# Optimization experiments

Measured on AMD Instinct MI355X. Metric: run time of the kernel, lower is better.

The kernel has to match this reference:

```python
import jax, jax.numpy as jnp
import numpy as np

IN_DIM = 1024
OUT_DIM = 1024
NUM_HEADS = 16
DEPTH = IN_DIM // NUM_HEADS  # 64


def setup_inputs() -> dict:
    key = jax.random.key(0)
    ks = jax.random.split(key, 11)
    B, S = 8, 1024  # S must equal IN_DIM (reshape constraint in original module)
    s_in = 1.0 / np.sqrt(IN_DIM)
    return {
        "query": jax.random.normal(ks[0], (B, S, IN_DIM), jnp.float32),
        "key": jax.random.normal(ks[1], (B, S, IN_DIM), jnp.float32),
        "value": jax.random.normal(ks[2], (B, S, IN_DIM), jnp.float32),
        "Wq": jax.random.normal(ks[3], (IN_DIM, IN_DIM), jnp.float32) * s_in,
        "bq": jnp.zeros((IN_DIM,), jnp.float32),
        "Wk": jax.random.normal(ks[4], (IN_DIM, IN_DIM), jnp.float32) * s_in,
        "bk": jnp.zeros((IN_DIM,), jnp.float32),
        "Wv": jax.random.normal(ks[5], (IN_DIM, IN_DIM), jnp.float32) * s_in,
        "bv": jnp.zeros((IN_DIM,), jnp.float32),
        "Wo": jax.random.normal(ks[6], (OUT_DIM, IN_DIM), jnp.float32) * s_in,
        "bo": jnp.zeros((OUT_DIM,), jnp.float32),
    }


def reference(query, key, value, Wq, bq, Wk, bk, Wv, bv, Wo, bo):
    B, S, D = query.shape
    H, P = NUM_HEADS, DEPTH

    def split_heads(x):
        # (B,S,D) -> (B,S,H,P) -> transpose last two dims -> (B,S,P,H)
        return x.reshape(B, S, H, P).swapaxes(-1, -2)

    Q = split_heads(query @ Wq.T + bq)   # (B,S,P,H)
    K = split_heads(key @ Wk.T + bk)     # (B,S,P,H)
    V = split_heads(value @ Wv.T + bv)   # (B,S,P,H)

    scale = jnp.sqrt(jnp.float32(P))
    # scores over the depth axis, per (batch, token): (B,S,P,P)
    scores = jnp.einsum('bsph,bsqh->bspq', Q, K) / scale
    # original uses softmax over dim=0 (the batch axis) - reproduce faithfully
    attn = jax.nn.softmax(scores, axis=0)
    out = jnp.einsum('bspq,bsqh->bsph', attn, V)   # (B,S,P,H)
    # transpose(-1,-2) -> (B,S,H,P), reshape to (B,S,S) (requires H*P == S)
    out = out.swapaxes(-1, -2).reshape(B, S, S)
    out = out @ Wo.T + bo                           # (B,S,OUT_DIM)
    return jax.nn.sigmoid(out)
```

## Files before the change

### kernel.cpp

```cpp
#include <hip/hip_runtime.h>


using short8   = __attribute__((ext_vector_type(8))) short;
using floatx4  = __attribute__((ext_vector_type(4))) float;
using floatx16 = __attribute__((ext_vector_type(16))) float;

__device__ __forceinline__ float bf2f(unsigned short u) {
    return __uint_as_float(((unsigned)u) << 16);
}
__device__ __forceinline__ unsigned short f2bf(float f) {
    unsigned u = __float_as_uint(f);
    u += 0x7fffu + ((u >> 16) & 1u);
    return (unsigned short)(u >> 16);
}
__device__ __forceinline__ unsigned pack_trunc(float f0, float f1) {
    return __builtin_amdgcn_perm(__float_as_uint(f1), __float_as_uint(f0), 0x07060302u);
}
__device__ __forceinline__ unsigned pack_rne(float f0, float f1) {
    return (unsigned)f2bf(f0) | ((unsigned)f2bf(f1) << 16);
}
__device__ __forceinline__ void async_ld16(const void* g, void* l) {
    __builtin_amdgcn_global_load_lds(
        (const __attribute__((address_space(1))) unsigned int*)g,
        (__attribute__((address_space(3))) unsigned int*)l, 16, 0, 0);
}
__device__ __forceinline__ short8 lds_read_b128(unsigned addr) {
    short8 r;
    asm volatile("ds_read_b128 %0, %1" : "=v"(r) : "v"(addr));
    return r;
}

__device__ __forceinline__ void conv8(const float* src, unsigned short* d, size_t i) {
    float4 a = *(const float4*)(src + i);
    float4 b = *(const float4*)(src + i + 4);
    uint4 o;
    o.x = pack_rne(a.x, a.y);
    o.y = pack_rne(a.z, a.w);
    o.z = pack_rne(b.x, b.y);
    o.w = pack_rne(b.z, b.w);
    *(uint4*)(d + i) = o;
}

__global__ __launch_bounds__(256) void convert_weights(
    const float* __restrict__ w0, const float* __restrict__ w1,
    const float* __restrict__ w2, const float* __restrict__ w3,
    unsigned short* __restrict__ dst)
{
    const float* srcs[4] = {w0, w1, w2, w3};
    conv8(srcs[blockIdx.y], dst + (size_t)blockIdx.y * (1024u * 1024u),
          ((size_t)blockIdx.x * 256 + threadIdx.x) * 8);
}

__global__ __launch_bounds__(256) void convert_acts(
    const float* __restrict__ a0, const float* __restrict__ a1,
    const float* __restrict__ a2, unsigned short* __restrict__ dst)
{
    const float* srcs[3] = {a0, a1, a2};
    conv8(srcs[blockIdx.y], dst + (size_t)blockIdx.y * ((size_t)8192 * 1024),
          ((size_t)blockIdx.x * 256 + threadIdx.x) * 8);
}

template<bool AF32, bool SIG>
__global__ __launch_bounds__(256) void gemm128(
    const void* __restrict__ A0, const void* __restrict__ A1, const void* __restrict__ A2,
    const unsigned short* __restrict__ W0, const unsigned short* __restrict__ W1,
    const unsigned short* __restrict__ W2,
    const float* __restrict__ b0, const float* __restrict__ b1, const float* __restrict__ b2,
    void* __restrict__ C0, void* __restrict__ C1, void* __restrict__ C2)
{
    const int z = blockIdx.z;
    const void* Ap = (z == 0) ? A0 : (z == 1) ? A1 : A2;
    const unsigned short* W = (z == 0) ? W0 : (z == 1) ? W1 : W2;
    const float* bias = (z == 0) ? b0 : (z == 1) ? b1 : b2;
    void* Cp = (z == 0) ? C0 : (z == 1) ? C1 : C2;

    constexpr int Kd = 1024, Nd = 1024;
    const int t = threadIdx.x;
    const int w = t >> 6, lane = t & 63;
    const int l15 = lane & 15, quad = lane >> 4;
    const int blockM = blockIdx.x * 128;
    const int blockN = blockIdx.y * 128;
    const int wy = w >> 1, wx = w & 1;

    __shared__ unsigned short Bs[128 * 32];
    constexpr int ABYTES = AF32 ? (128 * 32 * 4) : (128 * 32 * 2);
    __shared__ __align__(16) unsigned char AsRaw[ABYTES];
    float* AsF = (float*)AsRaw;
    unsigned short* AsB = (unsigned short*)AsRaw;

    const int br  = lane >> 2;
    const int bg  = (lane & 3) ^ (br & 3);
    const unsigned short* Bsrc0 = W + (size_t)(blockN + w * 32 + br) * Kd + bg * 8;
    const unsigned short* Bsrc1 = Bsrc0 + (size_t)16 * Kd;
    unsigned short* Bdst0 = &Bs[(w * 2 + 0) * 512];
    unsigned short* Bdst1 = &Bs[(w * 2 + 1) * 512];

    const int ar = lane >> 3;
    const int ag = (lane & 7) ^ (ar & 7);
    const float* AsrcF[4];
    float* AdstF[4];
    const unsigned short* AsrcB0 = nullptr; const unsigned short* AsrcB1 = nullptr;
    unsigned short* AdstB0 = nullptr; unsigned short* AdstB1 = nullptr;
    if (AF32) {
        #pragma unroll
        for (int j = 0; j < 4; ++j) {
            AsrcF[j] = (const float*)Ap + (size_t)(blockM + w * 32 + j * 8 + ar) * Kd + ag * 4;
            AdstF[j] = AsF + (w * 4 + j) * 256;
        }
    } else {
        AsrcB0 = (const unsigned short*)Ap + (size_t)(blockM + w * 32 + br) * Kd + bg * 8;
        AsrcB1 = AsrcB0 + (size_t)16 * Kd;
        AdstB0 = &AsB[(w * 2 + 0) * 512];
        AdstB1 = &AsB[(w * 2 + 1) * 512];
    }

    floatx4 acc[4][4] = {};

    for (int k0 = 0; k0 < Kd; k0 += 32) {
        if (AF32) {
            #pragma unroll
            for (int j = 0; j < 4; ++j) async_ld16(AsrcF[j] + k0, AdstF[j]);
        } else {
            async_ld16(AsrcB0 + k0, AdstB0);
            async_ld16(AsrcB1 + k0, AdstB1);
        }
        async_ld16(Bsrc0 + k0, Bdst0);
        async_ld16(Bsrc1 + k0, Bdst1);
        __syncthreads();

        short8 af[4], bfr[4];
        #pragma unroll
        for (int mt = 0; mt < 4; ++mt) {
            const int row = wy * 64 + mt * 16 + l15;
            if (AF32) {
                const int r7 = l15 & 7;
                const float* ap = AsF + row * 32;
                float4 lo = *(const float4*)(ap + (((quad * 2 + 0) ^ r7) * 4));
                float4 hi = *(const float4*)(ap + (((quad * 2 + 1) ^ r7) * 4));
                union { unsigned u[4]; short8 s; } cv;
                cv.u[0] = pack_rne(lo.x, lo.y);
                cv.u[1] = pack_rne(lo.z, lo.w);
                cv.u[2] = pack_rne(hi.x, hi.y);
                cv.u[3] = pack_rne(hi.z, hi.w);
                af[mt] = cv.s;
            } else {
                af[mt] = *(const short8*)&AsB[row * 32 + (quad ^ (l15 & 3)) * 8];
            }
        }
        #pragma unroll
        for (int nt = 0; nt < 4; ++nt) {
            const int row = wx * 64 + nt * 16 + l15;
            bfr[nt] = *(const short8*)&Bs[row * 32 + (quad ^ (l15 & 3)) * 8];
        }
        #pragma unroll
        for (int mt = 0; mt < 4; ++mt)
            #pragma unroll
            for (int nt = 0; nt < 4; ++nt)
                acc[mt][nt] = __builtin_amdgcn_mfma_f32_16x16x32_bf16(af[mt], bfr[nt], acc[mt][nt], 0, 0, 0);
        __syncthreads();
    }

    #pragma unroll
    for (int nt = 0; nt < 4; ++nt) {
        const int col = blockN + wx * 64 + nt * 16 + l15;
        const float bv = bias[col];
        #pragma unroll
        for (int mt = 0; mt < 4; ++mt) {
            const int row = blockM + wy * 64 + mt * 16 + quad * 4;
            #pragma unroll
            for (int r = 0; r < 4; ++r) {
                float v = acc[mt][nt][r] + bv;
                if (SIG) {
                    v = 1.0f / (1.0f + __expf(-v));
                    ((float*)Cp)[(size_t)(row + r) * Nd + col] = v;
                } else {
                    ((unsigned short*)Cp)[(size_t)(row + r) * Nd + col] = f2bf(v);
                }
            }
        }
    }
}

#define VMW10 do { asm volatile("s_waitcnt vmcnt(10)" ::: "memory"); } while (0)
#define VMW8  do { asm volatile("s_waitcnt vmcnt(8)"  ::: "memory"); } while (0)
#define VMW4  do { asm volatile("s_waitcnt vmcnt(4)"  ::: "memory"); } while (0)
#define VMW0  do { asm volatile("s_waitcnt vmcnt(0)"  ::: "memory"); } while (0)
#define LGKM0 do { asm volatile("s_waitcnt lgkmcnt(0)" ::: "memory"); \
                   __builtin_amdgcn_sched_barrier(0); } while (0)
#define BARRIER __builtin_amdgcn_s_barrier()

#define STG_A(BUF, KH, KE) do { \
    async_ld16(pA[0] + (KE), &lds[(BUF)*32768 + (KH)*16384 + dstW]); \
    async_ld16(pA[1] + (KE), &lds[(BUF)*32768 + (KH)*16384 + 8192 + dstW]); \
} while (0)
#define STG_B(BUF, KH, KE) do { \
    async_ld16(pB[0] + (KE), &lds[65536 + (BUF)*32768 + (KH)*16384 + dstW]); \
    async_ld16(pB[1] + (KE), &lds[65536 + (BUF)*32768 + (KH)*16384 + 8192 + dstW]); \
} while (0)

#define RD_A(BUF, KH, MH) do { \
    const unsigned rbA_ = (BUF)*32768u + (KH)*16384u; \
    aF[0][0] = lds_read_b128(aRd[(MH)*2+0][0] + rbA_); \
    aF[0][1] = lds_read_b128(aRd[(MH)*2+0][1] + rbA_); \
    aF[1][0] = lds_read_b128(aRd[(MH)*2+1][0] + rbA_); \
    aF[1][1] = lds_read_b128(aRd[(MH)*2+1][1] + rbA_); \
} while (0)
#define RD_B(BUF, KH) do { \
    const unsigned rbB_ = (BUF)*32768u + (KH)*16384u; \
    bF[0][0] = lds_read_b128(bRd[0][0] + rbB_); \
    bF[0][1] = lds_read_b128(bRd[0][1] + rbB_); \
    bF[1][0] = lds_read_b128(bRd[1][0] + rbB_); \
    bF[1][1] = lds_read_b128(bRd[1][1] + rbB_); \
} while (0)
#define MM(MH) do { \
    _Pragma("unroll") \
    for (int ks_ = 0; ks_ < 2; ++ks_) \
      _Pragma("unroll") \
      for (int af_ = 0; af_ < 2; ++af_) \
        _Pragma("unroll") \
        for (int nf_ = 0; nf_ < 2; ++nf_) \
          acc[(MH)*2+af_][nf_] = __builtin_amdgcn_mfma_f32_32x32x16_bf16( \
              aF[af_][ks_], bF[nf_][ks_], acc[(MH)*2+af_][nf_], 0, 0, 0); \
} while (0)

template<bool SIG>
__global__ __launch_bounds__(512, 2) void gemm8p(
    const unsigned short* __restrict__ A0, const unsigned short* __restrict__ A1,
    const unsigned short* __restrict__ A2,
    const unsigned short* __restrict__ W0, const unsigned short* __restrict__ W1,
    const unsigned short* __restrict__ W2,
    const float* __restrict__ b0, const float* __restrict__ b1, const float* __restrict__ b2,
    void* __restrict__ C0, void* __restrict__ C1, void* __restrict__ C2)
{
    const int z = blockIdx.z;
    const unsigned short* A = (z == 0) ? A0 : (z == 1) ? A1 : A2;
    const unsigned short* W = (z == 0) ? W0 : (z == 1) ? W1 : W2;
    const float* bias = (z == 0) ? b0 : (z == 1) ? b1 : b2;
    void* Cp = (z == 0) ? C0 : (z == 1) ? C1 : C2;

    const int t = threadIdx.x;
    const int w = t >> 6, l = t & 63;
    const int wy = w >> 2, wx = w & 3;
    const int l31 = l & 31, h5 = l >> 5;
    const int blockM = blockIdx.x * 256;
    const int blockN = blockIdx.y * 256;

    __shared__ __align__(16) unsigned char lds[131072];

    const unsigned ldsBase = (unsigned)(size_t)&lds[0];
    const int swz = (l31 >> 1) & 3;
    unsigned aRd[4][2], bRd[2][2];
    #pragma unroll
    for (int mf = 0; mf < 4; ++mf)
        #pragma unroll
        for (int ks = 0; ks < 2; ++ks)
            aRd[mf][ks] = ldsBase + (unsigned)((wy * 128 + mf * 32 + l31) * 64)
                          + (unsigned)((((ks * 2 + h5) ^ swz)) * 16);
    #pragma unroll
    for (int nf = 0; nf < 2; ++nf)
        #pragma unroll
        for (int ks = 0; ks < 2; ++ks)
            bRd[nf][ks] = ldsBase + 65536u + (unsigned)((wx * 64 + nf * 32 + l31) * 64)
                          + (unsigned)((((ks * 2 + h5) ^ swz)) * 16);

    const unsigned short* pA[2];
    const unsigned short* pB[2];
    #pragma unroll
    for (int i = 0; i < 2; ++i) {
        const int q = i * 512 + t;
        const int r = q >> 2;
        const int g = (q & 3) ^ ((r >> 1) & 3);
        pA[i] = A + (size_t)(blockM + r) * 1024 + g * 8;
        pB[i] = W + (size_t)(blockN + r) * 1024 + g * 8;
    }
    const int dstW = w * 1024;

    short8 aF[2][2], bF[2][2];
    floatx16 acc[4][2] = {};

    STG_B(0, 0, 0);  STG_A(0, 0, 0);
    STG_B(0, 1, 32); STG_A(0, 1, 32);
    STG_B(1, 0, 64); STG_A(1, 0, 64);
    STG_B(1, 1, 96);
    VMW10;
    BARRIER;

    #pragma unroll 1
    for (int i = 0; i < 7; ++i) {
        const int kb = i * 128;
        RD_A(0,0,0); RD_B(0,0); STG_A(1,1, kb +  96); LGKM0; MM(0);        BARRIER;
        RD_A(0,0,1);            STG_B(0,0, kb + 128); LGKM0; MM(1); VMW10; BARRIER;
        RD_A(0,1,0); RD_B(0,1); STG_A(0,0, kb + 128); LGKM0; MM(0);        BARRIER;
        RD_A(0,1,1);            STG_B(0,1, kb + 160); LGKM0; MM(1); VMW10; BARRIER;
        RD_A(1,0,0); RD_B(1,0); STG_A(0,1, kb + 160); LGKM0; MM(0);        BARRIER;
        RD_A(1,0,1);            STG_B(1,0, kb + 192); LGKM0; MM(1); VMW10; BARRIER;
        RD_A(1,1,0); RD_B(1,1); STG_A(1,0, kb + 192); LGKM0; MM(0);        BARRIER;
        RD_A(1,1,1);            STG_B(1,1, kb + 224); LGKM0; MM(1); VMW10; BARRIER;
    }
    RD_A(0,0,0); RD_B(0,0); STG_A(1,1, 992); LGKM0; MM(0);        BARRIER;
    RD_A(0,0,1);                             LGKM0; MM(1); VMW8;  BARRIER;
    RD_A(0,1,0); RD_B(0,1);                  LGKM0; MM(0);        BARRIER;
    RD_A(0,1,1);                             LGKM0; MM(1); VMW4;  BARRIER;
    RD_A(1,0,0); RD_B(1,0);                  LGKM0; MM(0);        BARRIER;
    RD_A(1,0,1);                             LGKM0; MM(1); VMW0;  BARRIER;
    RD_A(1,1,0); RD_B(1,1);                  LGKM0; MM(0);        BARRIER;
    RD_A(1,1,1);                             LGKM0; MM(1);

    const int colBase = blockN + wx * 64 + l31;
    const float bv0 = bias[colBase];
    const float bv1 = bias[colBase + 32];
    #pragma unroll
    for (int mf = 0; mf < 4; ++mf) {
        const int row0 = blockM + wy * 128 + mf * 32 + h5 * 4;
        #pragma unroll
        for (int nf = 0; nf < 2; ++nf) {
            const float bb = nf ? bv1 : bv0;
            const int col = colBase + nf * 32;
            #pragma unroll
            for (int rg = 0; rg < 16; ++rg) {
                const int row = row0 + (rg & 3) + 8 * (rg >> 2);
                float v = acc[mf][nf][rg] + bb;
                if (SIG) {
                    v = 1.0f / (1.0f + __expf(-v));
                    ((float*)Cp)[(size_t)row * 1024 + col] = v;
                } else {
                    ((unsigned short*)Cp)[(size_t)row * 1024 + col] = f2bf(v);
                }
            }
        }
    }
}

__global__ __launch_bounds__(512) void attn_mfma(
    const unsigned short* __restrict__ Q,
    const unsigned short* __restrict__ Kt,
    const unsigned short* __restrict__ Vt,
    unsigned short* __restrict__ O2)
{
    constexpr int VOFF = 0;
    constexpr int UOFF = 9216;
    constexpr int QOFF = UOFF + 8192;
    __shared__ __align__(16) unsigned short lds[UOFF + 18432];

    const int s  = blockIdx.x;
    const int ph = blockIdx.y;
    const int t  = threadIdx.x;
    const int w  = t >> 6;
    const int l  = t & 63;
    const int l15 = l & 15, l31 = l & 31, half = l >> 5, quad = l >> 4;

    const size_t gb = ((size_t)w * 1024 + s) * 1024;

    {
        const unsigned* vg = (const unsigned*)(Vt + gb);
        unsigned* vd = (unsigned*)lds;
        #pragma unroll
        for (int it = 0; it < 8; ++it) {
            const int h = it * 2 + half;
            vd[w * 576 + h * 36 + l31] = vg[h * 32 + l31];
        }
        const unsigned short* kg = Kt + gb;
        unsigned* kd = (unsigned*)(lds + UOFF);
        #pragma unroll
        for (int h2 = 0; h2 < 8; ++h2) {
            unsigned klo = kg[(2 * h2) * 64 + l];
            unsigned khi = kg[(2 * h2 + 1) * 64 + l];
            kd[w * 512 + l * 8 + h2] = klo | (khi << 16);
        }
        const unsigned short* qg = Q + gb + ph * 32;
        unsigned* qd = (unsigned*)(lds + QOFF);
        #pragma unroll
        for (int it = 0; it < 4; ++it) {
            const int h = it * 4 + half * 2;
            unsigned qlo = qg[h * 64 + l31];
            unsigned qhi = qg[(h + 1) * 64 + l31];
            qd[w * 256 + l31 * 8 + it * 2 + half] = qlo | (qhi << 16);
        }
    }
    __syncthreads();

    floatx16 sc[2];
    {
        short8 qf = *(const short8*)&lds[QOFF + w * 512 + l31 * 16 + half * 8];
        short8 kf0 = *(const short8*)&lds[UOFF + w * 1024 + l31 * 16 + half * 8];
        short8 kf1 = *(const short8*)&lds[UOFF + w * 1024 + (32 + l31) * 16 + half * 8];
        floatx16 z = {};
        sc[0] = __builtin_amdgcn_mfma_f32_32x32x16_bf16(kf0, qf, z, 0, 0, 0);
        sc[1] = __builtin_amdgcn_mfma_f32_32x32x16_bf16(kf1, qf, z, 0, 0, 0);
    }
    __syncthreads();

    {
        unsigned short* sx = lds + UOFF + w * 2304 + l31 * 72;
        #pragma unroll
        for (int nt = 0; nt < 2; ++nt) {
            #pragma unroll
            for (int rg = 0; rg < 4; ++rg) {
                float e0 = __expf(sc[nt][4 * rg + 0] * 0.125f);
                float e1 = __expf(sc[nt][4 * rg + 1] * 0.125f);
                float e2 = __expf(sc[nt][4 * rg + 2] * 0.125f);
                float e3 = __expf(sc[nt][4 * rg + 3] * 0.125f);
                uint2 pk = { pack_trunc(e0, e1), pack_trunc(e2, e3) };
                const int q0 = nt * 32 + rg * 8 + half * 4;
                *(uint2*)&sx[q0] = pk;
            }
        }
    }
    __syncthreads();

    {
        const int p  = t & 31;
        const int q0 = (t >> 5) * 4;
        unsigned short* base = lds + UOFF + p * 72 + q0;
        float fv[8][4];
        float den0 = 0.f, den1 = 0.f, den2 = 0.f, den3 = 0.f;
        #pragma unroll
        for (int b = 0; b < 8; ++b) {
            uint2 v = *(const uint2*)&base[b * 2304];
            fv[b][0] = bf2f((unsigned short)(v.x & 0xffff));
            fv[b][1] = bf2f((unsigned short)(v.x >> 16));
            fv[b][2] = bf2f((unsigned short)(v.y & 0xffff));
            fv[b][3] = bf2f((unsigned short)(v.y >> 16));
            den0 += fv[b][0]; den1 += fv[b][1]; den2 += fv[b][2]; den3 += fv[b][3];
        }
        const float r0 = __builtin_amdgcn_rcpf(den0);
        const float r1 = __builtin_amdgcn_rcpf(den1);
        const float r2 = __builtin_amdgcn_rcpf(den2);
        const float r3 = __builtin_amdgcn_rcpf(den3);
        #pragma unroll
        for (int b = 0; b < 8; ++b) {
            uint2 pk = { pack_trunc(fv[b][0] * r0, fv[b][1] * r1),
                         pack_trunc(fv[b][2] * r2, fv[b][3] * r3) };
            *(uint2*)&base[b * 2304] = pk;
        }
    }
    __syncthreads();

    floatx4 o[2] = {};
    #pragma unroll
    for (int qc = 0; qc < 2; ++qc) {
        short8 vf = *(const short8*)&lds[VOFF + w * 1152 + l15 * 72 + qc * 32 + quad * 8];
        #pragma unroll
        for (int mt = 0; mt < 2; ++mt) {
            short8 wf = *(const short8*)&lds[UOFF + w * 2304 + (mt * 16 + l15) * 72 + qc * 32 + quad * 8];
            o[mt] = __builtin_amdgcn_mfma_f32_16x16x32_bf16(wf, vf, o[mt], 0, 0, 0);
        }
    }
    {
        unsigned short* ol = lds + UOFF + w * 2304 + l15 * 36;
        #pragma unroll
        for (int mt = 0; mt < 2; ++mt) {
            uint2 pk = { pack_trunc(o[mt][0], o[mt][1]), pack_trunc(o[mt][2], o[mt][3]) };
            *(uint2*)&ol[mt * 16 + quad * 4] = pk;
        }
    }
    __syncthreads();

    {
        unsigned* outdw = (unsigned*)O2;
        const unsigned* ol = (const unsigned*)(lds + UOFF + w * 2304);
        const size_t gdw = ((size_t)w * 1024 + s) * 512 + ph * 16;
        #pragma unroll
        for (int i = 0; i < 4; ++i) {
            const int d = i * 64 + l;
            const int h = d >> 4, pq = d & 15;
            outdw[gdw + h * 32 + pq] = ol[h * 18 + pq];
        }
    }
}

extern "C" void kernel_launch(void* const* d_in, const int* in_sizes, int n_in,
                              void* d_out, int out_size, void* d_ws, size_t ws_size,
                              hipStream_t stream) {
    const float* query = (const float*)d_in[0];
    const float* key_  = (const float*)d_in[1];
    const float* value = (const float*)d_in[2];
    const float* Wq = (const float*)d_in[3];
    const float* bq = (const float*)d_in[4];
    const float* Wk = (const float*)d_in[5];
    const float* bk = (const float*)d_in[6];
    const float* Wv = (const float*)d_in[7];
    const float* bv = (const float*)d_in[8];
    const float* Wo = (const float*)d_in[9];
    const float* bo = (const float*)d_in[10];

    const size_t WN = (size_t)1024 * 1024;
    const size_t MN = (size_t)8192 * 1024;

    unsigned short* Wbf = (unsigned short*)d_ws;
    unsigned short* Wq_bf = Wbf;
    unsigned short* Wk_bf = Wbf + WN;
    unsigned short* Wv_bf = Wbf + 2 * WN;
    unsigned short* Wo_bf = Wbf + 3 * WN;

    convert_weights<<<dim3(512, 4), dim3(256), 0, stream>>>(Wq, Wk, Wv, Wo, Wbf);

    const bool big = ws_size >= (4 * WN + 6 * MN) * sizeof(unsigned short);

    unsigned short* Qb; unsigned short* Kb; unsigned short* Vb;
    if (big) {
        unsigned short* abf = Wbf + 4 * WN;
        Qb = abf + 3 * MN; Kb = Qb + MN; Vb = Kb + MN;
        convert_acts<<<dim3(4096, 3), dim3(256), 0, stream>>>(query, key_, value, abf);
        gemm8p<false><<<dim3(32, 4, 3), dim3(512), 0, stream>>>(
            abf, abf + MN, abf + 2 * MN, Wq_bf, Wk_bf, Wv_bf, bq, bk, bv, Qb, Kb, Vb);
    } else {
        Qb = Wbf + 4 * WN; Kb = Qb + MN; Vb = Kb + MN;
        gemm128<true, false><<<dim3(64, 8, 3), dim3(256), 0, stream>>>(
            query, key_, value, Wq_bf, Wk_bf, Wv_bf, bq, bk, bv, Qb, Kb, Vb);
    }

    unsigned short* O2 = Qb;
    attn_mfma<<<dim3(1024, 2), dim3(512), 0, stream>>>(Qb, Kb, Vb, O2);

    gemm8p<true><<<dim3(32, 4, 1), dim3(512), 0, stream>>>(
        O2, O2, O2, Wo_bf, Wo_bf, Wo_bf, bo, bo, bo, d_out, d_out, d_out);
}
```

Baseline: 281.6 us.

## Add 128x256-tile GEMM with two blocks per CU for output projection

Adds a new gemm4p kernel using 128x256 tiles, a 2-deep double-buffered async global-to-LDS pipeline, swizzled LDS, and launch bounds of 512 threads with 2 blocks per CU. It replaces the larger-tile gemm8p for the final output projection, doubling the grid to 256 blocks. The goal is better CU occupancy and latency hiding for the single 8192x1024x1024 GEMM, which previously launched only 128 blocks. The trade-off is less data reuse per block and a new hand-written vmcnt schedule that must be correct.

```diff
diff --git a/kernel.cpp b/kernel.cpp
--- a/kernel.cpp
+++ b/kernel.cpp
@@ -183,7 +183,9 @@
 
 #define VMW10 do { asm volatile("s_waitcnt vmcnt(10)" ::: "memory"); } while (0)
 #define VMW8  do { asm volatile("s_waitcnt vmcnt(8)"  ::: "memory"); } while (0)
+#define VMW6  do { asm volatile("s_waitcnt vmcnt(6)"  ::: "memory"); } while (0)
 #define VMW4  do { asm volatile("s_waitcnt vmcnt(4)"  ::: "memory"); } while (0)
+#define VMW3  do { asm volatile("s_waitcnt vmcnt(3)"  ::: "memory"); } while (0)
 #define VMW0  do { asm volatile("s_waitcnt vmcnt(0)"  ::: "memory"); } while (0)
 #define LGKM0 do { asm volatile("s_waitcnt lgkmcnt(0)" ::: "memory"); \
                    __builtin_amdgcn_sched_barrier(0); } while (0)
@@ -331,6 +333,129 @@
     }
 }
 
+#define STG4(BUF, KH, KE) do { \
+    async_ld16(pA4 + (KE), &lds[(BUF)*16384 + (KH)*8192 + dstW4]); \
+    async_ld16(pB4[0] + (KE), &lds[32768 + (BUF)*32768 + (KH)*16384 + dstW4]); \
+    async_ld16(pB4[1] + (KE), &lds[32768 + (BUF)*32768 + (KH)*16384 + 8192 + dstW4]); \
+} while (0)
+
+#define RD4(BUF, KH) do { \
+    const unsigned ra_ = (BUF)*16384u + (KH)*8192u; \
+    const unsigned rb_ = (BUF)*32768u + (KH)*16384u; \
+    aF[0][0] = lds_read_b128(aRd4[0][0] + ra_); \
+    aF[0][1] = lds_read_b128(aRd4[0][1] + ra_); \
+    aF[1][0] = lds_read_b128(aRd4[1][0] + ra_); \
+    aF[1][1] = lds_read_b128(aRd4[1][1] + ra_); \
+    bF[0][0] = lds_read_b128(bRd4[0][0] + rb_); \
+    bF[0][1] = lds_read_b128(bRd4[0][1] + rb_); \
+    bF[1][0] = lds_read_b128(bRd4[1][0] + rb_); \
+    bF[1][1] = lds_read_b128(bRd4[1][1] + rb_); \
+} while (0)
+
+#define MM4 do { \
+    _Pragma("unroll") \
+    for (int ks_ = 0; ks_ < 2; ++ks_) \
+      _Pragma("unroll") \
+      for (int mf_ = 0; mf_ < 2; ++mf_) \
+        _Pragma("unroll") \
+        for (int nf_ = 0; nf_ < 2; ++nf_) \
+          acc[mf_][nf_] = __builtin_amdgcn_mfma_f32_32x32x16_bf16( \
+              aF[mf_][ks_], bF[nf_][ks_], acc[mf_][nf_], 0, 0, 0); \
+} while (0)
+
+template<bool SIG>
+__global__ __launch_bounds__(512, 2) void gemm4p(
+    const unsigned short* __restrict__ A,
+    const unsigned short* __restrict__ W,
+    const float* __restrict__ bias,
+    void* __restrict__ Cp)
+{
+    const int t = threadIdx.x;
+    const int w = t >> 6, l = t & 63;
+    const int wy = w >> 2, wx = w & 3;
+    const int l31 = l & 31, h5 = l >> 5;
+    const int blockM = blockIdx.x * 128;
+    const int blockN = blockIdx.y * 256;
+
+    __shared__ __align__(16) unsigned char lds[98304];
+
+    const unsigned ldsBase = (unsigned)(size_t)&lds[0];
+    const int swz = (l31 >> 1) & 3;
+    unsigned aRd4[2][2], bRd4[2][2];
+    #pragma unroll
+    for (int mf = 0; mf < 2; ++mf)
+        #pragma unroll
+        for (int ks = 0; ks < 2; ++ks)
+            aRd4[mf][ks] = ldsBase + (unsigned)((wy * 64 + mf * 32 + l31) * 64)
+                           + (unsigned)((((ks * 2 + h5) ^ swz)) * 16);
+    #pragma unroll
+    for (int nf = 0; nf < 2; ++nf)
+        #pragma unroll
+        for (int ks = 0; ks < 2; ++ks)
+            bRd4[nf][ks] = ldsBase + 32768u + (unsigned)((wx * 64 + nf * 32 + l31) * 64)
+                           + (unsigned)((((ks * 2 + h5) ^ swz)) * 16);
+
+    const unsigned short* pA4;
+    {
+        const int r = t >> 2;
+        const int g = (t & 3) ^ ((r >> 1) & 3);
+        pA4 = A + (size_t)(blockM + r) * 1024 + g * 8;
+    }
+    const unsigned short* pB4[2];
+    #pragma unroll
+    for (int i = 0; i < 2; ++i) {
+        const int q = i * 512 + t;
+        const int r = q >> 2;
+        const int g = (q & 3) ^ ((r >> 1) & 3);
+        pB4[i] = W + (size_t)(blockN + r) * 1024 + g * 8;
+    }
+    const int dstW4 = w * 1024;
+
+    short8 aF[2][2], bF[2][2];
+    floatx16 acc[2][2] = {};
+
+    STG4(0, 0, 0); STG4(0, 1, 32); STG4(1, 0, 64);
+    VMW6;
+    BARRIER;
+
+    #pragma unroll 1
+    for (int i = 0; i < 7; ++i) {
+        const int kb = i * 128;
+        RD4(0,0); STG4(1,1, kb +  96); LGKM0; MM4; VMW6; BARRIER;
+        RD4(0,1); STG4(0,0, kb + 128); LGKM0; MM4; VMW6; BARRIER;
+        RD4(1,0); STG4(0,1, kb + 160); LGKM0; MM4; VMW6; BARRIER;
+        RD4(1,1); STG4(1,0, kb + 192); LGKM0; MM4; VMW6; BARRIER;
+    }
+    RD4(0,0); STG4(1,1, 992); LGKM0; MM4; VMW6; BARRIER;
+    RD4(0,1);                 LGKM0; MM4; VMW3; BARRIER;
+    RD4(1,0);                 LGKM0; MM4; VMW0; BARRIER;
+    RD4(1,1);                 LGKM0; MM4;
+
+    const int colBase = blockN + wx * 64 + l31;
+    const float bv0 = bias[colBase];
+    const float bv1 = bias[colBase + 32];
+    #pragma unroll
+    for (int mf = 0; mf < 2; ++mf) {
+        const int row0 = blockM + wy * 64 + mf * 32 + h5 * 4;
+        #pragma unroll
+        for (int nf = 0; nf < 2; ++nf) {
+            const float bb = nf ? bv1 : bv0;
+            const int col = colBase + nf * 32;
+            #pragma unroll
+            for (int rg = 0; rg < 16; ++rg) {
+                const int row = row0 + (rg & 3) + 8 * (rg >> 2);
+                float v = acc[mf][nf][rg] + bb;
+                if (SIG) {
+                    v = 1.0f / (1.0f + __expf(-v));
+                    ((float*)Cp)[(size_t)row * 1024 + col] = v;
+                } else {
+                    ((unsigned short*)Cp)[(size_t)row * 1024 + col] = f2bf(v);
+                }
+            }
+        }
+    }
+}
+
 __global__ __launch_bounds__(512) void attn_mfma(
     const unsigned short* __restrict__ Q,
     const unsigned short* __restrict__ Kt,
@@ -513,6 +638,5 @@
     unsigned short* O2 = Qb;
     attn_mfma<<<dim3(1024, 2), dim3(512), 0, stream>>>(Qb, Kb, Vb, O2);
 
-    gemm8p<true><<<dim3(32, 4, 1), dim3(512), 0, stream>>>(
-        O2, O2, O2, Wo_bf, Wo_bf, Wo_bf, bo, bo, bo, d_out, d_out, d_out);
-}
+    gemm4p<true><<<dim3(64, 4), dim3(512), 0, stream>>>(O2, Wo_bf, bo, (float*)d_out);
+}
```

Result: faster. 272.3 us (-3.3%).
